# Kernel tuning notes

Hardware: AMD Instinct MI355X
Metric: run time of the kernel (lower is better)

## Reference

```python
import jax, jax.numpy as jnp
import numpy as np

B_BLK = 64      # sparse_block_size
LOCAL = 4       # sparse_local_num_blocks
GLOB = 2        # sparse_global_num_blocks
STRIDE = 4      # sparse_global_block_stride
NH = 16
NKV = 4
HD = 128
SCALE = HD ** -0.5
NEG = -1e9


def _build_block_index(num_blocks):
    """Static per-query-block key-block index table + validity mask."""
    max_sel = LOCAL + 1 + GLOB
    idx = np.zeros((num_blocks, max_sel), np.int32)
    valid = np.zeros((num_blocks, max_sel), bool)
    for t in range(num_blocks):
        local = list(range(max(0, t - LOCAL), t + 1))
        cand = list(range(0, t + 1, max(1, STRIDE)))
        glob = cand[-GLOB:] if (GLOB > 0 and len(cand) > 0) else []
        sel = sorted(set(local + glob))
        idx[t, :len(sel)] = sel
        valid[t, :len(sel)] = True
    return idx, valid


def _rotate_half(x):
    x1, x2 = jnp.split(x, 2, axis=-1)
    return jnp.concatenate((-x2, x1), axis=-1)


def setup_inputs() -> dict:
    key = jax.random.key(0)
    ks = jax.random.split(key, 7)
    bsz, S, H = 1, 4096, 2048
    return {
        "hidden_states": jax.random.normal(ks[0], (bsz, S, H), jnp.float32) * 0.02,
        "cos": jax.random.uniform(ks[1], (bsz, S, HD), jnp.float32, -1.0, 1.0),
        "sin": jax.random.uniform(ks[2], (bsz, S, HD), jnp.float32, -1.0, 1.0),
        "wq": jax.random.normal(ks[3], (NH * HD, H), jnp.float32) * 0.02,
        "wk": jax.random.normal(ks[4], (NKV * HD, H), jnp.float32) * 0.02,
        "wv": jax.random.normal(ks[5], (NKV * HD, H), jnp.float32) * 0.02,
        "wo": jax.random.normal(ks[6], (H, NH * HD), jnp.float32) * 0.02,
    }


def reference(hidden_states, cos, sin, wq, wk, wv, wo):
    b, S, H = hidden_states.shape
    # QKV projections (nn.Linear: x @ W.T), split heads -> [b, h, S, d]
    q = (hidden_states @ wq.T).reshape(b, S, NH, HD).transpose(0, 2, 1, 3)
    k = (hidden_states @ wk.T).reshape(b, S, NKV, HD).transpose(0, 2, 1, 3)
    v = (hidden_states @ wv.T).reshape(b, S, NKV, HD).transpose(0, 2, 1, 3)
    # RoPE (cos/sin broadcast over heads)
    c = cos[:, None, :, :]
    s = sin[:, None, :, :]
    q = q * c + _rotate_half(q) * s
    k = k * c + _rotate_half(k) * s
    # GQA: repeat KV heads
    n_rep = NH // NKV
    k = jnp.repeat(k, n_rep, axis=1)
    v = jnp.repeat(v, n_rep, axis=1)
    # Block-sparse local+global attention (S divisible by B_BLK -> no padding)
    T = S // B_BLK
    q_blk = q.reshape(b, NH, T, B_BLK, HD)
    k_blk = k.reshape(b, NH, T, B_BLK, HD)
    v_blk = v.reshape(b, NH, T, B_BLK, HD)
    idx, valid = _build_block_index(T)           # [T, Smax] static
    Smax = idx.shape[1]
    k_sel = k_blk[:, :, idx]                     # [b,h,T,Smax,Bk,d]
    v_sel = v_blk[:, :, idx]
    scores = jnp.einsum('bhtqd,bhtspd->bhtqsp', q_blk, k_sel) * SCALE
    # causal intra-block mask on the diagonal block, -inf on padded slots
    intra = jnp.triu(jnp.full((B_BLK, B_BLK), NEG, jnp.float32), 1)
    is_diag = jnp.asarray(idx == np.arange(T)[:, None], jnp.float32)  # [T,Smax]
    mask = is_diag[:, None, :, None] * intra[None, :, None, :]        # [T,Bq,Smax,Bk]
    mask = mask + jnp.where(jnp.asarray(valid)[:, None, :, None], 0.0, NEG)
    scores = scores + mask[None, None]
    scores = scores.reshape(b, NH, T, B_BLK, Smax * B_BLK)
    probs = jax.nn.softmax(scores, axis=-1)
    out = jnp.einsum('bhtqk,bhtkd->bhtqd', probs,
                     v_sel.reshape(b, NH, T, Smax * B_BLK, HD))
    out = out.reshape(b, NH, S, HD).transpose(0, 2, 1, 3).reshape(b, S, NH * HD)
    return out @ wo.T
```

## Files before the change

### kernel.cpp

```cpp
#include <hip/hip_runtime.h>

typedef unsigned short u16;
typedef short bf16x8 __attribute__((ext_vector_type(8)));
typedef float f32x4 __attribute__((ext_vector_type(4)));

#define S_LEN 4096
#define NHEADS 16
#define NKVH 4
#define HDIM 128
#define HID 2048
#define NQKV 3072

__device__ __forceinline__ u16 f2bf(float x) {
  union { float f; unsigned u; } v; v.f = x;
  unsigned r = v.u + 0x7fffu + ((v.u >> 16) & 1u);
  return (u16)(r >> 16);
}
__device__ __forceinline__ float bf2f(u16 x) {
  union { unsigned u; float f; } v; v.u = ((unsigned)x) << 16;
  return v.f;
}
__device__ __forceinline__ void async16(u16* lds, const u16* g) {
  __builtin_amdgcn_global_load_lds((const __attribute__((address_space(1))) void*)g,
                                   (__attribute__((address_space(3))) void*)lds, 16, 0, 0);
}

__global__ __launch_bounds__(256) void cast_f32_bf16(const float* __restrict__ in,
                                                     u16* __restrict__ out, int n4) {
  int i = blockIdx.x * 256 + threadIdx.x;
  if (i >= n4) return;
  float4 v = ((const float4*)in)[i];
  ushort4 o;
  o.x = f2bf(v.x); o.y = f2bf(v.y); o.z = f2bf(v.z); o.w = f2bf(v.w);
  ((ushort4*)out)[i] = o;
}

template<bool OUT_BF16>
__global__ __launch_bounds__(256) void gemm_bt(const u16* __restrict__ A, const u16* __restrict__ B,
                                               void* __restrict__ Cp, int M, int N, int K) {
  __shared__ __align__(16) u16 As[128 * 64];
  __shared__ __align__(16) u16 Bs[128 * 64];
  const int tid = threadIdx.x;
  const int w = tid >> 6, l = tid & 63;
  const int quad = l >> 4, l16 = l & 15;
  const int bm = blockIdx.x, bn = blockIdx.y;
  const int wr = w & 1, wc = w >> 1;

  const size_t abase = (size_t)bm * 128 * K;
  const size_t bbase = (size_t)bn * 128 * K;

  f32x4 acc[4][4];
  for (int i = 0; i < 4; ++i)
    for (int j = 0; j < 4; ++j) acc[i][j] = f32x4{0.f, 0.f, 0.f, 0.f};

  int sm[4], sc[4];
  for (int j = 0; j < 4; ++j) {
    int slot = (w * 4 + j) * 64 + l;
    sm[j] = slot >> 3;
    sc[j] = (slot & 7) ^ (sm[j] & 7);
  }
  int aoff[2][4], boff[2][4];
  for (int ksi = 0; ksi < 2; ++ksi) {
    int cb = ksi * 4 + quad;
    for (int mt = 0; mt < 4; ++mt) {
      int m = wr * 64 + mt * 16 + l16;
      aoff[ksi][mt] = (m * 8 + (cb ^ (m & 7))) * 8;
      int n = wc * 64 + mt * 16 + l16;
      boff[ksi][mt] = (n * 8 + (cb ^ (n & 7))) * 8;
    }
  }

  for (int kt = 0; kt < K; kt += 64) {
    __syncthreads();
    for (int j = 0; j < 4; ++j) {
      async16(&As[(w * 4 + j) * 64 * 8], A + abase + (size_t)sm[j] * K + kt + sc[j] * 8);
      async16(&Bs[(w * 4 + j) * 64 * 8], B + bbase + (size_t)sm[j] * K + kt + sc[j] * 8);
    }
    __syncthreads();
    for (int ksi = 0; ksi < 2; ++ksi) {
      bf16x8 af[4], bv[4];
      for (int mt = 0; mt < 4; ++mt) {
        af[mt] = *(const bf16x8*)&As[aoff[ksi][mt]];
        bv[mt] = *(const bf16x8*)&Bs[boff[ksi][mt]];
      }
      for (int mt = 0; mt < 4; ++mt)
        for (int nt = 0; nt < 4; ++nt)
          acc[mt][nt] = __builtin_amdgcn_mfma_f32_16x16x32_bf16(af[mt], bv[nt], acc[mt][nt], 0, 0, 0);
    }
  }

  const int row_base = bm * 128 + wr * 64;
  const int col_base = bn * 128 + wc * 64;
  for (int mt = 0; mt < 4; ++mt)
    for (int nt = 0; nt < 4; ++nt) {
      int col = col_base + nt * 16 + l16;
      for (int r = 0; r < 4; ++r) {
        int row = row_base + mt * 16 + quad * 4 + r;
        float v = acc[mt][nt][r];
        if (OUT_BF16) ((u16*)Cp)[(size_t)row * N + col] = f2bf(v);
        else          ((float*)Cp)[(size_t)row * N + col] = v;
      }
    }
}

#define VMC4 asm volatile("s_waitcnt vmcnt(4)" ::: "memory")
#define VMC0 asm volatile("s_waitcnt vmcnt(0)" ::: "memory")
#define NOVM ((void)0)

#define STAGE_A(buf, h, kt) do { \
    async16(&As[buf][adst[h][0]], asrc[h][0] + (size_t)(kt) * 64); \
    async16(&As[buf][adst[h][1]], asrc[h][1] + (size_t)(kt) * 64); \
  } while (0)
#define STAGE_B(buf, h, kt) do { \
    async16(&Bs[buf][bdst[h][0]], bsrc[h][0] + (size_t)(kt) * 64); \
    async16(&Bs[buf][bdst[h][1]], bsrc[h][1] + (size_t)(kt) * 64); \
  } while (0)

#define PHASE(cur, mh, nh, STAGE_STMT, VM) do { \
    bf16x8 af_[4][2], bf_[2][2]; \
    _Pragma("unroll") \
    for (int i_ = 0; i_ < 4; ++i_) { \
      const int m64_ = (wm * 128 + ((mh) * 4 + i_) * 16 + l16) * 64; \
      af_[i_][0] = *(const bf16x8*)&As[cur][m64_ + ((quad ^ x7) * 8)]; \
      af_[i_][1] = *(const bf16x8*)&As[cur][m64_ + (((4 + quad) ^ x7) * 8)]; \
    } \
    _Pragma("unroll") \
    for (int i_ = 0; i_ < 2; ++i_) { \
      const int n64_ = (wn * 64 + ((nh) * 2 + i_) * 16 + l16) * 64; \
      bf_[i_][0] = *(const bf16x8*)&Bs[cur][n64_ + ((quad ^ x7) * 8)]; \
      bf_[i_][1] = *(const bf16x8*)&Bs[cur][n64_ + (((4 + quad) ^ x7) * 8)]; \
    } \
    STAGE_STMT; \
    __builtin_amdgcn_s_barrier(); \
    asm volatile("s_waitcnt lgkmcnt(0)" ::: "memory"); \
    __builtin_amdgcn_sched_barrier(0); \
    __builtin_amdgcn_s_setprio(1); \
    _Pragma("unroll") \
    for (int ks_ = 0; ks_ < 2; ++ks_) \
      _Pragma("unroll") \
      for (int i_ = 0; i_ < 4; ++i_) \
        _Pragma("unroll") \
        for (int j_ = 0; j_ < 2; ++j_) \
          acc[(mh) * 4 + i_][(nh) * 2 + j_] = __builtin_amdgcn_mfma_f32_16x16x32_bf16( \
              af_[i_][ks_], bf_[j_][ks_], acc[(mh) * 4 + i_][(nh) * 2 + j_], 0, 0, 0); \
    __builtin_amdgcn_s_setprio(0); \
    VM; \
    __builtin_amdgcn_s_barrier(); \
  } while (0)

template<bool OUT_BF16>
__global__ __launch_bounds__(512, 2) void gemm8p(const u16* __restrict__ A, const u16* __restrict__ B,
                                                 void* __restrict__ Cp, int M, int N, int K) {
  __shared__ __align__(16) u16 As[2][256 * 64];
  __shared__ __align__(16) u16 Bs[2][256 * 64];
  const int tid = threadIdx.x;
  const int w = tid >> 6, l = tid & 63, quad = l >> 4, l16 = l & 15;
  const int wm = w >> 2, wn = w & 3;
  const int x7 = l16 & 7;
  const int bm = blockIdx.x, bn = blockIdx.y;

  const u16* asrc[2][2]; int adst[2][2];
  const u16* bsrc[2][2]; int bdst[2][2];
#pragma unroll
  for (int h = 0; h < 2; ++h)
#pragma unroll
    for (int j = 0; j < 2; ++j) {
      int u = j * 512 + w * 64 + l;
      int r = u >> 3, cc = u & 7;
      int ma = ((r >> 6) << 7) + (h << 6) + (r & 63);
      asrc[h][j] = A + (size_t)(bm * 256 + ma) * K + (size_t)((cc ^ (ma & 7)) * 8);
      int nb = ((r >> 5) << 6) + (h << 5) + (r & 31);
      bsrc[h][j] = B + (size_t)(bn * 256 + nb) * K + (size_t)((cc ^ (nb & 7)) * 8);
      int r0 = j * 64 + w * 8;
      adst[h][j] = (((r0 >> 6) << 7) + (h << 6) + (r0 & 63)) * 64;
      bdst[h][j] = (((r0 >> 5) << 6) + (h << 5) + (r0 & 31)) * 64;
    }

  f32x4 acc[8][4];
#pragma unroll
  for (int i = 0; i < 8; ++i)
#pragma unroll
    for (int j = 0; j < 4; ++j) acc[i][j] = f32x4{0.f, 0.f, 0.f, 0.f};

  STAGE_A(0, 0, 0); STAGE_B(0, 0, 0); STAGE_B(0, 1, 0); STAGE_A(0, 1, 0);
  STAGE_A(1, 0, 1); STAGE_B(1, 0, 1);
  VMC4;
  __builtin_amdgcn_s_barrier();

  const int NI = K >> 7;
  for (int it = 0; it < NI; ++it) {
    const int t1 = 2 * it + 1, t2 = 2 * it + 2, t3 = 2 * it + 3;
    const bool full = (it + 1 < NI);
    PHASE(0, 0, 0, STAGE_B(1, 1, t1), NOVM);
    PHASE(0, 0, 1, STAGE_A(1, 1, t1), NOVM);
    PHASE(0, 1, 0, if (full) STAGE_A(0, 0, t2), NOVM);
    PHASE(0, 1, 1, if (full) STAGE_B(0, 0, t2), if (full) VMC4; else VMC0);
    PHASE(1, 0, 0, if (full) STAGE_B(0, 1, t2), NOVM);
    PHASE(1, 0, 1, if (full) STAGE_A(0, 1, t2), NOVM);
    PHASE(1, 1, 0, if (full) STAGE_A(1, 0, t3), NOVM);
    PHASE(1, 1, 1, if (full) STAGE_B(1, 0, t3), if (full) VMC4);
  }

  const int row0 = bm * 256 + wm * 128;
  const int col0 = bn * 256 + wn * 64;
#pragma unroll
  for (int mf = 0; mf < 8; ++mf)
#pragma unroll
    for (int nf = 0; nf < 4; ++nf) {
      const int col = col0 + nf * 16 + l16;
#pragma unroll
      for (int r = 0; r < 4; ++r) {
        const int row = row0 + mf * 16 + quad * 4 + r;
        float v = acc[mf][nf][r];
        if (OUT_BF16) ((u16*)Cp)[(size_t)row * N + col] = f2bf(v);
        else          ((float*)Cp)[(size_t)row * N + col] = v;
      }
    }
}

__global__ __launch_bounds__(256) void rope_scatter(const u16* __restrict__ qkv,
                                                    const float* __restrict__ cosp,
                                                    const float* __restrict__ sinp,
                                                    u16* __restrict__ Q, u16* __restrict__ Kd) {
  int idx = blockIdx.x * 256 + threadIdx.x;
  int d = idx & 63;
  int hh = (idx >> 6) % 20;
  int s = idx / (20 * 64);
  size_t base = (size_t)s * NQKV + hh * 128;
  float x1 = bf2f(qkv[base + d]);
  float x2 = bf2f(qkv[base + d + 64]);
  float c1 = cosp[s * 128 + d], s1 = sinp[s * 128 + d];
  float c2 = cosp[s * 128 + d + 64], s2 = sinp[s * 128 + d + 64];
  float o1 = x1 * c1 - x2 * s1;
  float o2 = x2 * c2 + x1 * s2;
  u16* dst = (hh < NHEADS) ? (Q + ((size_t)hh * S_LEN + s) * HDIM)
                           : (Kd + ((size_t)(hh - NHEADS) * S_LEN + s) * HDIM);
  dst[d] = f2bf(o1);
  dst[d + 64] = f2bf(o2);
}

__global__ __launch_bounds__(256) void vtrans(const u16* __restrict__ qkv, u16* __restrict__ Vt) {
  __shared__ u16 tile[64][65];
  int s0 = blockIdx.x * 64;
  int j0 = blockIdx.y * 64;
  int tid = threadIdx.x;
  for (int it = 0; it < 16; ++it) {
    int lin = it * 256 + tid;
    int sr = lin >> 6, jc = lin & 63;
    tile[sr][jc] = qkv[(size_t)(s0 + sr) * NQKV + 2560 + j0 + jc];
  }
  __syncthreads();
  for (int it = 0; it < 16; ++it) {
    int lin = it * 256 + tid;
    int dr = lin >> 6, sc = lin & 63;
    Vt[(size_t)(j0 + dr) * S_LEN + s0 + sc] = tile[sc][dr];
  }
}

__global__ __launch_bounds__(256) void attn_kernel(const u16* __restrict__ Q, const u16* __restrict__ K,
                                                   const u16* __restrict__ Vt, u16* __restrict__ Aout) {
  const float SCALE = 0.08838834764831845f;
  const float NEGF = -3.0e38f;
  const int t = blockIdx.x, h = blockIdx.y;
  const int kvh = h >> 2;
  const int tid = threadIdx.x;
  const int w = tid >> 6, l = tid & 63, quad = l >> 4, l16 = l & 15;

  __shared__ __align__(16) u16 Qs[64 * 128];
  __shared__ __align__(16) u16 Ks[64 * 128];
  __shared__ __align__(16) u16 Vs[128 * 64];
  __shared__ __align__(16) u16 Ps[4 * 16 * 72];

  int sel[7]; int nsel = 0;
  {
    int g1 = (t >> 2) << 2, g0 = g1 - 4;
    int lo = t - 4; if (lo < 0) lo = 0;
    if (g0 >= 0 && g0 < lo) sel[nsel++] = g0;
    if (g1 < lo) sel[nsel++] = g1;
    for (int b = lo; b <= t; ++b) sel[nsel++] = b;
  }

  {
    const size_t qbase = ((size_t)h * S_LEN + t * 64) * HDIM;
    for (int j = 0; j < 4; ++j) {
      int slot = (w * 4 + j) * 64 + l;
      int m = slot >> 4;
      int c = (slot & 15) ^ (m & 15);
      async16(&Qs[(w * 4 + j) * 64 * 8], Q + qbase + m * 128 + c * 8);
    }
  }

  float m_run[4], l_run[4];
  for (int r = 0; r < 4; ++r) { m_run[r] = NEGF; l_run[r] = 0.f; }
  f32x4 oacc[8];
  for (int i = 0; i < 8; ++i) oacc[i] = f32x4{0.f, 0.f, 0.f, 0.f};

  for (int ib = 0; ib < nsel; ++ib) {
    const int kb = sel[ib];
    __syncthreads();
    {
      const size_t kbase = ((size_t)kvh * S_LEN + kb * 64) * HDIM;
      const size_t vbase = (size_t)kvh * HDIM * S_LEN + kb * 64;
      for (int j = 0; j < 4; ++j) {
        int slot = (w * 4 + j) * 64 + l;
        int mk = slot >> 4;
        int ck = (slot & 15) ^ (mk & 15);
        async16(&Ks[(w * 4 + j) * 64 * 8], K + kbase + mk * 128 + ck * 8);
        int dv = slot >> 3;
        int cv = (slot & 7) ^ (dv & 7);
        async16(&Vs[(w * 4 + j) * 64 * 8], Vt + vbase + (size_t)dv * S_LEN + cv * 8);
      }
    }
    __syncthreads();

    f32x4 sacc[4];
    for (int nt = 0; nt < 4; ++nt) sacc[nt] = f32x4{0.f, 0.f, 0.f, 0.f};
    const int mq = w * 16 + l16;
    for (int ks = 0; ks < 128; ks += 32) {
      int cb = (ks >> 3) + quad;
      bf16x8 af = *(const bf16x8*)&Qs[(mq * 16 + (cb ^ (mq & 15))) * 8];
      for (int nt = 0; nt < 4; ++nt) {
        int n = nt * 16 + l16;
        bf16x8 bv = *(const bf16x8*)&Ks[(n * 16 + (cb ^ (n & 15))) * 8];
        sacc[nt] = __builtin_amdgcn_mfma_f32_16x16x32_bf16(af, bv, sacc[nt], 0, 0, 0);
      }
    }

    const bool diag = (kb == t);
    float alpha[4];
    for (int r = 0; r < 4; ++r) {
      int qrow = w * 16 + quad * 4 + r;
      float pv[4];
      float vmax = NEGF;
      for (int nt = 0; nt < 4; ++nt) {
        float v = sacc[nt][r] * SCALE;
        if (diag && (nt * 16 + l16) > qrow) v = NEGF;
        pv[nt] = v;
        vmax = fmaxf(vmax, v);
      }
      for (int off = 1; off < 16; off <<= 1) vmax = fmaxf(vmax, __shfl_xor(vmax, off));
      float mnew = fmaxf(m_run[r], vmax);
      alpha[r] = __expf(m_run[r] - mnew);
      m_run[r] = mnew;
      float sum = 0.f;
      for (int nt = 0; nt < 4; ++nt) {
        float p = __expf(pv[nt] - mnew);
        sum += p;
        Ps[(w * 16 + quad * 4 + r) * 72 + nt * 16 + l16] = f2bf(p);
      }
      for (int off = 1; off < 16; off <<= 1) sum += __shfl_xor(sum, off);
      l_run[r] = l_run[r] * alpha[r] + sum;
    }
    for (int nt = 0; nt < 8; ++nt) {
      f32x4 o = oacc[nt];
      o[0] *= alpha[0]; o[1] *= alpha[1]; o[2] *= alpha[2]; o[3] *= alpha[3];
      oacc[nt] = o;
    }

    for (int ks = 0; ks < 64; ks += 32) {
      bf16x8 pf = *(const bf16x8*)&Ps[(w * 16 + l16) * 72 + ks + quad * 8];
      int cb = (ks >> 3) + quad;
      for (int nt = 0; nt < 8; ++nt) {
        int n = nt * 16 + l16;
        bf16x8 vv = *(const bf16x8*)&Vs[(n * 8 + (cb ^ (n & 7))) * 8];
        oacc[nt] = __builtin_amdgcn_mfma_f32_16x16x32_bf16(pf, vv, oacc[nt], 0, 0, 0);
      }
    }
  }

  float inv[4];
  for (int r = 0; r < 4; ++r) inv[r] = 1.f / l_run[r];
  const int srow = t * 64 + w * 16 + quad * 4;
  for (int nt = 0; nt < 8; ++nt) {
    int col = h * 128 + nt * 16 + l16;
    for (int r = 0; r < 4; ++r)
      Aout[(size_t)(srow + r) * HID + col] = f2bf(oacc[nt][r] * inv[r]);
  }
}

extern "C" void kernel_launch(void* const* d_in, const int* in_sizes, int n_in,
                              void* d_out, int out_size, void* d_ws, size_t ws_size,
                              hipStream_t stream) {
  const float* hs   = (const float*)d_in[0];
  const float* cosp = (const float*)d_in[1];
  const float* sinp = (const float*)d_in[2];
  const float* wq   = (const float*)d_in[3];
  const float* wk   = (const float*)d_in[4];
  const float* wv   = (const float*)d_in[5];
  const float* wo   = (const float*)d_in[6];

  u16* hsb = (u16*)d_ws;
  u16* W   = hsb + (size_t)S_LEN * HID;
  u16* wob = W + (size_t)NQKV * HID;
  u16* qkv = wob + (size_t)HID * HID;
  u16* Qm  = qkv + (size_t)S_LEN * NQKV;
  u16* Km  = Qm + (size_t)NHEADS * S_LEN * HDIM;
  u16* Vt  = Km + (size_t)NKVH * S_LEN * HDIM;
  u16* att = Vt + (size_t)NKVH * HDIM * S_LEN;

  cast_f32_bf16<<<8192, 256, 0, stream>>>(hs, hsb, 2097152);
  cast_f32_bf16<<<4096, 256, 0, stream>>>(wq, W, 1048576);
  cast_f32_bf16<<<1024, 256, 0, stream>>>(wk, W + (size_t)4194304, 262144);
  cast_f32_bf16<<<1024, 256, 0, stream>>>(wv, W + (size_t)5242880, 262144);
  cast_f32_bf16<<<4096, 256, 0, stream>>>(wo, wob, 1048576);

  gemm8p<true><<<dim3(16, 12), 512, 0, stream>>>(hsb, W, (void*)qkv, 4096, 3072, 2048);
  rope_scatter<<<20480, 256, 0, stream>>>(qkv, cosp, sinp, Qm, Km);
  vtrans<<<dim3(64, 8), 256, 0, stream>>>(qkv, Vt);
  attn_kernel<<<dim3(64, 16), 256, 0, stream>>>(Qm, Km, Vt, att);
  gemm_bt<false><<<dim3(32, 16), 256, 0, stream>>>(att, wob, d_out, 4096, 2048, 2048);
}
```

Before: 305.3 us.

## Reuse LDS fragments across phases and use pipelined GEMM for output projection

Reorders the 8-phase GEMM so A and B fragments read from LDS are kept in registers and reused across consecutive phases (snake order over the sub-tiles), which roughly halves the LDS reads per iteration. Also removes the simple single-buffered 128x128 GEMM and runs the output projection with the double-buffered 256x256 gemm8p kernel. This adds register pressure, and the output GEMM now launches only 128 blocks, which may underfill the GPU.

```diff
diff --git a/kernel.cpp b/kernel.cpp
--- a/kernel.cpp
+++ b/kernel.cpp
@@ -35,74 +35,6 @@
   ((ushort4*)out)[i] = o;
 }
 
-template<bool OUT_BF16>
-__global__ __launch_bounds__(256) void gemm_bt(const u16* __restrict__ A, const u16* __restrict__ B,
-                                               void* __restrict__ Cp, int M, int N, int K) {
-  __shared__ __align__(16) u16 As[128 * 64];
-  __shared__ __align__(16) u16 Bs[128 * 64];
-  const int tid = threadIdx.x;
-  const int w = tid >> 6, l = tid & 63;
-  const int quad = l >> 4, l16 = l & 15;
-  const int bm = blockIdx.x, bn = blockIdx.y;
-  const int wr = w & 1, wc = w >> 1;
-
-  const size_t abase = (size_t)bm * 128 * K;
-  const size_t bbase = (size_t)bn * 128 * K;
-
-  f32x4 acc[4][4];
-  for (int i = 0; i < 4; ++i)
-    for (int j = 0; j < 4; ++j) acc[i][j] = f32x4{0.f, 0.f, 0.f, 0.f};
-
-  int sm[4], sc[4];
-  for (int j = 0; j < 4; ++j) {
-    int slot = (w * 4 + j) * 64 + l;
-    sm[j] = slot >> 3;
-    sc[j] = (slot & 7) ^ (sm[j] & 7);
-  }
-  int aoff[2][4], boff[2][4];
-  for (int ksi = 0; ksi < 2; ++ksi) {
-    int cb = ksi * 4 + quad;
-    for (int mt = 0; mt < 4; ++mt) {
-      int m = wr * 64 + mt * 16 + l16;
-      aoff[ksi][mt] = (m * 8 + (cb ^ (m & 7))) * 8;
-      int n = wc * 64 + mt * 16 + l16;
-      boff[ksi][mt] = (n * 8 + (cb ^ (n & 7))) * 8;
-    }
-  }
-
-  for (int kt = 0; kt < K; kt += 64) {
-    __syncthreads();
-    for (int j = 0; j < 4; ++j) {
-      async16(&As[(w * 4 + j) * 64 * 8], A + abase + (size_t)sm[j] * K + kt + sc[j] * 8);
-      async16(&Bs[(w * 4 + j) * 64 * 8], B + bbase + (size_t)sm[j] * K + kt + sc[j] * 8);
-    }
-    __syncthreads();
-    for (int ksi = 0; ksi < 2; ++ksi) {
-      bf16x8 af[4], bv[4];
-      for (int mt = 0; mt < 4; ++mt) {
-        af[mt] = *(const bf16x8*)&As[aoff[ksi][mt]];
-        bv[mt] = *(const bf16x8*)&Bs[boff[ksi][mt]];
-      }
-      for (int mt = 0; mt < 4; ++mt)
-        for (int nt = 0; nt < 4; ++nt)
-          acc[mt][nt] = __builtin_amdgcn_mfma_f32_16x16x32_bf16(af[mt], bv[nt], acc[mt][nt], 0, 0, 0);
-    }
-  }
-
-  const int row_base = bm * 128 + wr * 64;
-  const int col_base = bn * 128 + wc * 64;
-  for (int mt = 0; mt < 4; ++mt)
-    for (int nt = 0; nt < 4; ++nt) {
-      int col = col_base + nt * 16 + l16;
-      for (int r = 0; r < 4; ++r) {
-        int row = row_base + mt * 16 + quad * 4 + r;
-        float v = acc[mt][nt][r];
-        if (OUT_BF16) ((u16*)Cp)[(size_t)row * N + col] = f2bf(v);
-        else          ((float*)Cp)[(size_t)row * N + col] = v;
-      }
-    }
-}
-
 #define VMC4 asm volatile("s_waitcnt vmcnt(4)" ::: "memory")
 #define VMC0 asm volatile("s_waitcnt vmcnt(0)" ::: "memory")
 #define NOVM ((void)0)
@@ -116,20 +48,24 @@
     async16(&Bs[buf][bdst[h][1]], bsrc[h][1] + (size_t)(kt) * 64); \
   } while (0)
 
-#define PHASE(cur, mh, nh, STAGE_STMT, VM) do { \
-    bf16x8 af_[4][2], bf_[2][2]; \
+#define RD_A(cur, mh) do { \
     _Pragma("unroll") \
     for (int i_ = 0; i_ < 4; ++i_) { \
       const int m64_ = (wm * 128 + ((mh) * 4 + i_) * 16 + l16) * 64; \
-      af_[i_][0] = *(const bf16x8*)&As[cur][m64_ + ((quad ^ x7) * 8)]; \
-      af_[i_][1] = *(const bf16x8*)&As[cur][m64_ + (((4 + quad) ^ x7) * 8)]; \
-    } \
+      af[i_][0] = *(const bf16x8*)&As[cur][m64_ + ((quad ^ x7) * 8)]; \
+      af[i_][1] = *(const bf16x8*)&As[cur][m64_ + (((4 + quad) ^ x7) * 8)]; \
+    } } while (0)
+
+#define RD_B(cur, nh, dst) do { \
     _Pragma("unroll") \
-    for (int i_ = 0; i_ < 2; ++i_) { \
-      const int n64_ = (wn * 64 + ((nh) * 2 + i_) * 16 + l16) * 64; \
-      bf_[i_][0] = *(const bf16x8*)&Bs[cur][n64_ + ((quad ^ x7) * 8)]; \
-      bf_[i_][1] = *(const bf16x8*)&Bs[cur][n64_ + (((4 + quad) ^ x7) * 8)]; \
-    } \
+    for (int j_ = 0; j_ < 2; ++j_) { \
+      const int n64_ = (wn * 64 + ((nh) * 2 + j_) * 16 + l16) * 64; \
+      dst[j_][0] = *(const bf16x8*)&Bs[cur][n64_ + ((quad ^ x7) * 8)]; \
+      dst[j_][1] = *(const bf16x8*)&Bs[cur][n64_ + (((4 + quad) ^ x7) * 8)]; \
+    } } while (0)
+
+#define PH(READS, STAGE_STMT, MH, NH, BSET, VM) do { \
+    READS; \
     STAGE_STMT; \
     __builtin_amdgcn_s_barrier(); \
     asm volatile("s_waitcnt lgkmcnt(0)" ::: "memory"); \
@@ -141,8 +77,8 @@
       for (int i_ = 0; i_ < 4; ++i_) \
         _Pragma("unroll") \
         for (int j_ = 0; j_ < 2; ++j_) \
-          acc[(mh) * 4 + i_][(nh) * 2 + j_] = __builtin_amdgcn_mfma_f32_16x16x32_bf16( \
-              af_[i_][ks_], bf_[j_][ks_], acc[(mh) * 4 + i_][(nh) * 2 + j_], 0, 0, 0); \
+          acc[(MH) * 4 + i_][(NH) * 2 + j_] = __builtin_amdgcn_mfma_f32_16x16x32_bf16( \
+              af[i_][ks_], BSET[j_][ks_], acc[(MH) * 4 + i_][(NH) * 2 + j_], 0, 0, 0); \
     __builtin_amdgcn_s_setprio(0); \
     VM; \
     __builtin_amdgcn_s_barrier(); \
@@ -182,6 +118,8 @@
 #pragma unroll
     for (int j = 0; j < 4; ++j) acc[i][j] = f32x4{0.f, 0.f, 0.f, 0.f};
 
+  bf16x8 af[4][2], b0f[2][2], b1f[2][2];
+
   STAGE_A(0, 0, 0); STAGE_B(0, 0, 0); STAGE_B(0, 1, 0); STAGE_A(0, 1, 0);
   STAGE_A(1, 0, 1); STAGE_B(1, 0, 1);
   VMC4;
@@ -191,14 +129,14 @@
   for (int it = 0; it < NI; ++it) {
     const int t1 = 2 * it + 1, t2 = 2 * it + 2, t3 = 2 * it + 3;
     const bool full = (it + 1 < NI);
-    PHASE(0, 0, 0, STAGE_B(1, 1, t1), NOVM);
-    PHASE(0, 0, 1, STAGE_A(1, 1, t1), NOVM);
-    PHASE(0, 1, 0, if (full) STAGE_A(0, 0, t2), NOVM);
-    PHASE(0, 1, 1, if (full) STAGE_B(0, 0, t2), if (full) VMC4; else VMC0);
-    PHASE(1, 0, 0, if (full) STAGE_B(0, 1, t2), NOVM);
-    PHASE(1, 0, 1, if (full) STAGE_A(0, 1, t2), NOVM);
-    PHASE(1, 1, 0, if (full) STAGE_A(1, 0, t3), NOVM);
-    PHASE(1, 1, 1, if (full) STAGE_B(1, 0, t3), if (full) VMC4);
+    PH(RD_A(0, 0); RD_B(0, 0, b0f), STAGE_B(1, 1, t1),            0, 0, b0f, NOVM);
+    PH(RD_B(0, 1, b1f),             STAGE_A(1, 1, t1),            0, 1, b1f, NOVM);
+    PH(RD_A(0, 1),                  if (full) STAGE_A(0, 0, t2),  1, 1, b1f, NOVM);
+    PH(((void)0),                   if (full) STAGE_B(0, 0, t2),  1, 0, b0f, if (full) VMC4; else VMC0);
+    PH(RD_A(1, 0); RD_B(1, 0, b0f), if (full) STAGE_B(0, 1, t2),  0, 0, b0f, NOVM);
+    PH(RD_B(1, 1, b1f),             if (full) STAGE_A(0, 1, t2),  0, 1, b1f, NOVM);
+    PH(RD_A(1, 1),                  if (full) STAGE_A(1, 0, t3),  1, 1, b1f, NOVM);
+    PH(((void)0),                   if (full) STAGE_B(1, 0, t3),  1, 0, b0f, if (full) VMC4);
   }
 
   const int row0 = bm * 256 + wm * 128;
@@ -408,5 +346,5 @@
   rope_scatter<<<20480, 256, 0, stream>>>(qkv, cosp, sinp, Qm, Km);
   vtrans<<<dim3(64, 8), 256, 0, stream>>>(qkv, Vt);
   attn_kernel<<<dim3(64, 16), 256, 0, stream>>>(Qm, Km, Vt, att);
-  gemm_bt<false><<<dim3(32, 16), 256, 0, stream>>>(att, wob, d_out, 4096, 2048, 2048);
-}
+  gemm8p<false><<<dim3(16, 8), 512, 0, stream>>>(att, wob, d_out, 4096, 2048, 2048);
+}
```

After: 310.8 us. No clear change (+1.8%).
